# Optimization experiments

Measured on AMD Instinct MI355X. Metric: run time of the kernel, lower is better.

The kernel has to match this reference:

```python
import jax, jax.numpy as jnp
import numpy as np

N, FIN, FOUT, K = 4096, 512, 128, 4
LRELU_ALPHA = 0.2


def setup_inputs() -> dict:
    key = jax.random.key(0)
    k1, k2, k3, k4 = jax.random.split(key, 4)
    x = jax.random.normal(k1, (N, FIN), dtype=jnp.float32)
    # binary adjacency with guaranteed self-loops so every row has a neighbor
    adj = jax.random.randint(k2, (N, N), 0, 2, dtype=jnp.int32)
    adj = jnp.maximum(adj, jnp.eye(N, dtype=jnp.int32))
    # xavier-uniform-ish init for W:(K,FIN,FOUT) and a:(K,2*FOUT,1)
    limW = float(np.sqrt(6.0 / (FIN + FOUT)))
    W = jax.random.uniform(k3, (K, FIN, FOUT), dtype=jnp.float32, minval=-limW, maxval=limW)
    lima = float(np.sqrt(6.0 / (2 * FOUT + 1)))
    a = jax.random.uniform(k4, (K, 2 * FOUT, 1), dtype=jnp.float32, minval=-lima, maxval=lima)
    return {"x": x, "adj": adj, "W": W, "a": a}


def reference(x, adj, W, a):
    # x: [N, Fin], adj: [N, N] int, W: [K, Fin, F'], a: [K, 2F', 1]
    Fout = W.shape[-1]
    h = jnp.einsum('nf,kfo->nko', x, W)          # [N, K, F'] per-head projection
    a_src = a[:, :Fout, 0]                        # [K, F'] acts on h_i
    a_dst = a[:, Fout:, 0]                        # [K, F'] acts on h_j
    # a^T [h_i || h_j] == a_src . h_i + a_dst . h_j  (no O(N^2) concat)
    e_i = jnp.einsum('nko,ko->nk', h, a_src)      # [N, K]
    e_j = jnp.einsum('nko,ko->nk', h, a_dst)      # [N, K]
    scores = e_i[:, :, None] + e_j.T[None, :, :]  # [N, K, N]
    scores = jax.nn.leaky_relu(scores, LRELU_ALPHA)
    mask = (adj != 0)[:, None, :]                 # [N, 1, N]
    scores = jnp.where(mask, scores, -jnp.inf)
    coeffs = jax.nn.softmax(scores, axis=-1)      # [N, K, N]
    # dropout is identity in eval mode
    out = jnp.einsum('nkm,mko->nko', coeffs, h)   # [N, K, F'] aggregation
    return out.reshape(out.shape[0], -1)          # concat heads -> [N, K*F']
```

## Files before the change

kernel.cpp:

```cpp
#include <hip/hip_runtime.h>
#include <hip/hip_bf16.h>

typedef float f4 __attribute__((ext_vector_type(4)));
typedef int   i4 __attribute__((ext_vector_type(4)));
typedef unsigned short us8 __attribute__((ext_vector_type(8)));
typedef short bfrag __attribute__((ext_vector_type(8)));
typedef float f16v __attribute__((ext_vector_type(16)));

constexpr int NN   = 4096;
constexpr int FINc = 512;
constexpr int FOUTc= 128;
constexpr int KHc  = 4;
constexpr int KFc  = 512;
constexpr float ALPHA = 0.2f;
constexpr float LOG2E = 1.44269504088896340736f;

static __device__ __forceinline__ unsigned short f2bf(float f) {
    unsigned u = __float_as_uint(f);
    return (unsigned short)((u + 0x7fffu + ((u >> 16) & 1u)) >> 16);
}
static __device__ __forceinline__ float bf2f(unsigned short u) {
    return __uint_as_float(((unsigned)u) << 16);
}
static __device__ __forceinline__ bfrag us2bf(us8 v) {
    union { us8 u; bfrag s; } cv; cv.u = v; return cv.s;
}


__global__ __launch_bounds__(256) void prep_kernel(const float* __restrict__ x,
                                                   const float* __restrict__ W,
                                                   unsigned short* __restrict__ xb,
                                                   unsigned short* __restrict__ WbT) {
    __shared__ float tile[32 * 132];
    const int b = blockIdx.x, t = threadIdx.x;
    if (b < 1024) {
        size_t base = ((size_t)b * 256 + t) * 8;
        f4 v0 = *(const f4*)&x[base];
        f4 v1 = *(const f4*)&x[base + 4];
        us8 o;
#pragma unroll
        for (int j = 0; j < 4; ++j) { o[j] = f2bf(v0[j]); o[4 + j] = f2bf(v1[j]); }
        *(us8*)&xb[base] = o;
    } else {
        const int wb = b - 1024;
        const int k = wb >> 4, f0 = (wb & 15) * 32;
#pragma unroll
        for (int p = 0; p < 4; ++p) {
            int fl = p * 8 + (t >> 5);
            int oc = (t & 31) * 4;
            *(f4*)&tile[fl * 132 + oc] =
                *(const f4*)&W[(size_t)k * 65536 + (size_t)(f0 + fl) * 128 + oc];
        }
        __syncthreads();
        const int o = t >> 1, fh = (t & 1) * 16;
        alignas(16) unsigned short buf[16];
#pragma unroll
        for (int j = 0; j < 16; ++j) buf[j] = f2bf(tile[(fh + j) * 132 + o]);
        unsigned short* dst = &WbT[((size_t)k * 128 + o) * FINc + f0 + fh];
        *(us8*)dst       = *(const us8*)&buf[0];
        *(us8*)(dst + 8) = *(const us8*)&buf[8];
    }
}

__global__ __launch_bounds__(256) void gemmh_bits_kernel(const unsigned short* __restrict__ xb,
                                                         const unsigned short* __restrict__ WbT,
                                                         const int* __restrict__ adj,
                                                         unsigned short* __restrict__ hB,
                                                         unsigned* __restrict__ bits) {
    __shared__ char Ax[64 * 128];
    __shared__ char Bx[64 * 128];
    const int b = blockIdx.x, t = threadIdx.x;
    if (b >= 512) {
        size_t i0 = (size_t)(b - 512) * 16384 + (size_t)t * 64;
        const int* ap = adj + i0;
        unsigned long long bb = 0ull;
#pragma unroll
        for (int c = 0; c < 16; ++c) {
            i4 v = *(const i4*)(ap + c * 4);
            unsigned n = (v[0] != 0 ? 1u : 0u) | (v[1] != 0 ? 2u : 0u)
                       | (v[2] != 0 ? 4u : 0u) | (v[3] != 0 ? 8u : 0u);
            bb |= (unsigned long long)n << (c * 4);
        }
        *(unsigned long long*)&bits[i0 >> 5] = bb;
        return;
    }
    const int wid = t >> 6, lane = t & 63;
    const int c0 = (b & 7) * 64, n0 = (b >> 3) * 64;
    const int head = c0 >> 7, ob = c0 & 127;
    const int srow = t >> 2, sseg = t & 3;
    const unsigned short* asrc = &xb[(size_t)(n0 + srow) * FINc + sseg * 16];
    const unsigned short* bsrc = &WbT[((size_t)(head * 128 + ob + srow)) * FINc + sseg * 16];
    const int rowbase = (wid & 1) * 32, colbase = (wid >> 1) * 32;
    f16v acc = {};
    for (int fc = 0; fc < FINc; fc += 64) {
        us8 a0 = *(const us8*)(asrc + fc), a1 = *(const us8*)(asrc + fc + 8);
        us8 b0 = *(const us8*)(bsrc + fc), b1 = *(const us8*)(bsrc + fc + 8);
        __syncthreads();
        {
            int byt = (sseg * 32) ^ ((srow & 7) << 4);
            char* pa = Ax + srow * 128;
            *(us8*)(pa + byt) = a0;  *(us8*)(pa + (byt ^ 16)) = a1;
            char* pb = Bx + srow * 128;
            *(us8*)(pb + byt) = b0;  *(us8*)(pb + (byt ^ 16)) = b1;
        }
        __syncthreads();
#pragma unroll
        for (int ks = 0; ks < 4; ++ks) {
            int kb = ks * 32 + ((lane >> 5) << 4);
            int ar = rowbase + (lane & 31);
            bfrag af = *(const bfrag*)(Ax + ar * 128 + (kb ^ ((ar & 7) << 4)));
            int bc = colbase + (lane & 31);
            bfrag bf = *(const bfrag*)(Bx + bc * 128 + (kb ^ ((bc & 7) << 4)));
            acc = __builtin_amdgcn_mfma_f32_32x32x16_bf16(af, bf, acc, 0, 0, 0);
        }
    }
    __syncthreads();
#pragma unroll
    for (int reg = 0; reg < 16; ++reg) {
        int row = rowbase + (reg & 3) + 8 * (reg >> 2) + 4 * (lane >> 5);
        int col = colbase + (lane & 31);
        *(unsigned short*)(Ax + row * 128 + ((col * 2) ^ ((row & 7) << 4))) = f2bf(acc[reg]);
    }
    __syncthreads();
    {
        const int col_l = t & 63;
        unsigned short* dstbase = hB + (size_t)head * 524288 + (size_t)(n0 >> 6) * 8192
                                     + (size_t)(ob + col_l) * 8;
#pragma unroll
        for (int g = 0; g < 2; ++g) {
            int o8 = (t >> 6) + g * 4;
            int ks = o8 >> 1, lg = o8 & 1;
            alignas(16) unsigned short buf[8];
#pragma unroll
            for (int j = 0; j < 8; ++j) {
                int r = o8 * 8 + j;
                buf[j] = *(const unsigned short*)(Ax + r * 128 + ((col_l * 2) ^ ((r & 7) << 4)));
            }
            *(us8*)(dstbase + ks * 2048 + lg * 1024) = *(const us8*)buf;
        }
    }
}

__global__ __launch_bounds__(256) void e2_kernel(const unsigned short* __restrict__ hB,
                                                 const float* __restrict__ a,
                                                 float* __restrict__ ei,
                                                 float* __restrict__ ejT) {
    __shared__ unsigned short hs[8192];
    __shared__ float as[128], ad[128];
    __shared__ float pim[4][64], pjm[4][64];
    const int t = threadIdx.x;
    const int k = blockIdx.x >> 6;
    const int mc = blockIdx.x & 63;
    if (t < 128) as[t] = a[k * 256 + t] * LOG2E;
    else         ad[t - 128] = a[k * 256 + t] * LOG2E;
    const unsigned short* src = hB + ((size_t)k * 64 + mc) * 8192;
#pragma unroll
    for (int i = 0; i < 4; ++i) {
        int off = i * 2048 + t * 8;
        *(us8*)&hs[off] = *(const us8*)&src[off];
    }
    __syncthreads();
    const int m = t & 63, wq = t >> 6;
    const int base = (m >> 4) * 2048 + ((m >> 3) & 1) * 1024 + (m & 7);
    float si = 0.f, sj = 0.f;
#pragma unroll
    for (int cc = 0; cc < 32; ++cc) {
        int c = wq * 32 + cc;
        float v = bf2f(hs[base + c * 8]);
        si += v * as[c];
        sj += v * ad[c];
    }
    pim[wq][m] = si; pjm[wq][m] = sj;
    __syncthreads();
    if (t < 64) {
        ei[(mc * 64 + t) * KHc + k]        = pim[0][t] + pim[1][t] + pim[2][t] + pim[3][t];
        ejT[(size_t)k * NN + mc * 64 + t]  = pjm[0][t] + pjm[1][t] + pjm[2][t] + pjm[3][t];
    }
}

__global__ __launch_bounds__(256, 2) void out_mfma_kernel(const unsigned* __restrict__ bits,
                                                          const float* __restrict__ ei,
                                                          const float* __restrict__ ejT,
                                                          const unsigned short* __restrict__ hB,
                                                          float* __restrict__ out) {
    __shared__ unsigned bitsL[4][1056];
    __shared__ float ejred[4096];
    __shared__ float sred[4][32];
    __shared__ float lsum[32];
    const int bid = blockIdx.x;
    const int nb  = (bid & 7) * 64 + (bid >> 3);
    const int k   = nb >> 7;
    const int n0  = (nb & 127) * 32;
    const int t = threadIdx.x, lane = t & 63, w = t >> 6;
    const int row = lane & 31, kh = lane >> 5;
    const int mq  = w * 1024;
    {
        int r = lane >> 1, cb = (lane & 1) * 16;
        const unsigned* src = &bits[(size_t)(n0 + r) * 128 + (mq >> 5) + cb];
        unsigned* dst = &bitsL[w][r * 33 + cb];
#pragma unroll
        for (int c = 0; c < 16; ++c) dst[c] = src[c];
    }
    {
        const float* src = &ejT[(size_t)k * NN + mq + lane * 16];
        float* dst = &ejred[w * 1024 + lane * 16];
#pragma unroll
        for (int c = 0; c < 4; ++c) *(f4*)(dst + c * 4) = *(const f4*)(src + c * 4);
    }
    const float eiv = ei[(n0 + row) * KHc + k];
    const char* hbase = (const char*)hB + (size_t)k * 1048576 + (size_t)(mq >> 6) * 16384
                        + kh * 2048 + row * 16;
    bfrag ones;
#pragma unroll
    for (int j = 0; j < 8; ++j) ones[j] = (short)0x3F80;
    f16v acc0 = {}, acc1 = {}, acc2 = {}, acc3 = {}, accs = {};

    for (int it = 0; it < 16; ++it) {
        const char* hc = hbase + (size_t)it * 16384;
        unsigned bwA = bitsL[w][row * 33 + it * 2];
        unsigned bwB = bitsL[w][row * 33 + it * 2 + 1];
#pragma unroll
        for (int ks = 0; ks < 4; ++ks) {
            us8 hg0 = *(const us8*)(hc + ks * 4096);
            us8 hg1 = *(const us8*)(hc + ks * 4096 + 512);
            us8 hg2 = *(const us8*)(hc + ks * 4096 + 1024);
            us8 hg3 = *(const us8*)(hc + ks * 4096 + 1536);
            const int eb = w * 1024 + it * 64 + ks * 16 + kh * 8;
            f4 ej0 = *(const f4*)&ejred[eb];
            f4 ej1 = *(const f4*)&ejred[eb + 4];
            unsigned bw = ((ks & 2) ? bwB : bwA) >> ((ks & 1) * 16 + kh * 8);
            float p[8];
#pragma unroll
            for (int j = 0; j < 8; ++j) {
                float sc = eiv + (j < 4 ? ej0[j] : ej1[j - 4]);
                sc = fmaxf(sc, ALPHA * sc);
                float pp = exp2f(sc);
                p[j] = ((bw >> j) & 1) ? pp : 0.f;
            }
            union { unsigned u[4]; bfrag s; } pk;
#pragma unroll
            for (int j = 0; j < 4; ++j) {
                float2 fp; fp.x = p[2 * j]; fp.y = p[2 * j + 1];
                __hip_bfloat162 b2 = __float22bfloat162_rn(fp);
                pk.u[j] = *reinterpret_cast<unsigned*>(&b2);
            }
            acc0 = __builtin_amdgcn_mfma_f32_32x32x16_bf16(pk.s, us2bf(hg0), acc0, 0, 0, 0);
            acc1 = __builtin_amdgcn_mfma_f32_32x32x16_bf16(pk.s, us2bf(hg1), acc1, 0, 0, 0);
            acc2 = __builtin_amdgcn_mfma_f32_32x32x16_bf16(pk.s, us2bf(hg2), acc2, 0, 0, 0);
            acc3 = __builtin_amdgcn_mfma_f32_32x32x16_bf16(pk.s, us2bf(hg3), acc3, 0, 0, 0);
            accs = __builtin_amdgcn_mfma_f32_32x32x16_bf16(pk.s, ones, accs, 0, 0, 0);
        }
    }
    if (row == 0) {
#pragma unroll
        for (int reg = 0; reg < 16; ++reg) {
            int r = (reg & 3) + 8 * (reg >> 2) + 4 * kh;
            sred[w][r] = accs[reg];
        }
    }
    __syncthreads();
    if (t < 32) lsum[t] = 1.0f / ((sred[0][t] + sred[1][t]) + (sred[2][t] + sred[3][t]));
    float* red = ejred;
#pragma unroll
    for (int src = 1; src < 4; ++src) {
        if (w == src) {
#pragma unroll
            for (int cg = 0; cg < 4; ++cg) {
                const f16v& av = (cg == 0) ? acc0 : (cg == 1) ? acc1 : (cg == 2) ? acc2 : acc3;
#pragma unroll
                for (int reg = 0; reg < 16; ++reg) {
                    int r = (reg & 3) + 8 * (reg >> 2) + 4 * kh;
                    red[r * 128 + cg * 32 + row] = av[reg];
                }
            }
        }
        __syncthreads();
        if (w == 0) {
#pragma unroll
            for (int cg = 0; cg < 4; ++cg) {
                f16v& av = (cg == 0) ? acc0 : (cg == 1) ? acc1 : (cg == 2) ? acc2 : acc3;
#pragma unroll
                for (int reg = 0; reg < 16; ++reg) {
                    int r = (reg & 3) + 8 * (reg >> 2) + 4 * kh;
                    av[reg] += red[r * 128 + cg * 32 + row];
                }
            }
        }
        __syncthreads();
    }
    if (w == 0) {
#pragma unroll
        for (int cg = 0; cg < 4; ++cg) {
            const f16v& av = (cg == 0) ? acc0 : (cg == 1) ? acc1 : (cg == 2) ? acc2 : acc3;
#pragma unroll
            for (int reg = 0; reg < 16; ++reg) {
                int r = (reg & 3) + 8 * (reg >> 2) + 4 * kh;
                out[(size_t)(n0 + r) * KFc + k * FOUTc + cg * 32 + row] = av[reg] * lsum[r];
            }
        }
    }
}

extern "C" void kernel_launch(void* const* d_in, const int* in_sizes, int n_in,
                              void* d_out, int out_size, void* d_ws, size_t ws_size,
                              hipStream_t stream) {
    const float* x   = (const float*)d_in[0];
    const int*   adj = (const int*)d_in[1];
    const float* W   = (const float*)d_in[2];
    const float* a   = (const float*)d_in[3];
    float* out = (float*)d_out;
    char* ws = (char*)d_ws;

    unsigned short* hB   = (unsigned short*)ws;
    unsigned short* xb   = (unsigned short*)(ws + (4u << 20));
    unsigned short* WbT  = (unsigned short*)(ws + (20u << 20));
    unsigned*       bits = (unsigned*)(ws + (21u << 20));
    float*          ei   = (float*)(ws + (23u << 20));
    float*          ejT  = ei + (size_t)NN * KHc;

    prep_kernel<<<1088, 256, 0, stream>>>(x, W, xb, WbT);
    gemmh_bits_kernel<<<1536, 256, 0, stream>>>(xb, WbT, adj, hB, bits);
    e2_kernel<<<256, 256, 0, stream>>>(hB, a, ei, ejT);
    out_mfma_kernel<<<512, 256, 0, stream>>>(bits, ei, ejT, hB, out);
}
```

Baseline: 78.53 us.

## Factor leaky-relu exp into precomputed per-column terms and double waves per block

Rewrites exp2(leaky(ei+ej)) as max(exp2(ej), exp2(-0.8*ei)*exp2(0.2*ej)) up to a per-row factor that cancels in normalization. The per-column exponentials are computed once into shared memory, so the inner loop no longer evaluates an exp per element. The block also grows from 4 to 8 waves, each covering half as many columns, to add latency hiding, at the cost of a longer cross-wave reduction and more LDS. The factored form can overflow or lose precision when the ej values are large.

New measurement: 74.05 us. 1.06x faster.

```diff
diff --git a/kernel.cpp b/kernel.cpp
--- a/kernel.cpp
+++ b/kernel.cpp
@@ -12,7 +12,6 @@
 constexpr int FOUTc= 128;
 constexpr int KHc  = 4;
 constexpr int KFc  = 512;
-constexpr float ALPHA = 0.2f;
 constexpr float LOG2E = 1.44269504088896340736f;
 
 static __device__ __forceinline__ unsigned short f2bf(float f) {
@@ -178,14 +177,15 @@
     }
 }
 
-__global__ __launch_bounds__(256, 2) void out_mfma_kernel(const unsigned* __restrict__ bits,
+__global__ __launch_bounds__(512, 4) void out_mfma_kernel(const unsigned* __restrict__ bits,
                                                           const float* __restrict__ ei,
                                                           const float* __restrict__ ejT,
                                                           const unsigned short* __restrict__ hB,
                                                           float* __restrict__ out) {
-    __shared__ unsigned bitsL[4][1056];
-    __shared__ float ejred[4096];
-    __shared__ float sred[4][32];
+    __shared__ unsigned bitsL[8][544];
+    __shared__ float ejPL[4096];
+    __shared__ float ejNL[4096];
+    __shared__ float sred[8][32];
     __shared__ float lsum[32];
     const int bid = blockIdx.x;
     const int nb  = (bid & 7) * 64 + (bid >> 3);
@@ -193,21 +193,30 @@
     const int n0  = (nb & 127) * 32;
     const int t = threadIdx.x, lane = t & 63, w = t >> 6;
     const int row = lane & 31, kh = lane >> 5;
-    const int mq  = w * 1024;
+    const int mq  = w * 512;
     {
-        int r = lane >> 1, cb = (lane & 1) * 16;
+        int r = lane >> 1, cb = (lane & 1) * 8;
         const unsigned* src = &bits[(size_t)(n0 + r) * 128 + (mq >> 5) + cb];
-        unsigned* dst = &bitsL[w][r * 33 + cb];
-#pragma unroll
-        for (int c = 0; c < 16; ++c) dst[c] = src[c];
+        unsigned* dst = &bitsL[w][r * 17 + cb];
+#pragma unroll
+        for (int c = 0; c < 8; ++c) dst[c] = src[c];
     }
     {
-        const float* src = &ejT[(size_t)k * NN + mq + lane * 16];
-        float* dst = &ejred[w * 1024 + lane * 16];
-#pragma unroll
-        for (int c = 0; c < 4; ++c) *(f4*)(dst + c * 4) = *(const f4*)(src + c * 4);
+        const float* src = &ejT[(size_t)k * NN + mq + lane * 8];
+        f4 v0 = *(const f4*)src;
+        f4 v1 = *(const f4*)(src + 4);
+        float* dP = &ejPL[w * 512 + lane * 8];
+        float* dN = &ejNL[w * 512 + lane * 8];
+#pragma unroll
+        for (int c = 0; c < 4; ++c) {
+            dP[c]     = exp2f(v0[c]);
+            dP[c + 4] = exp2f(v1[c]);
+            dN[c]     = exp2f(0.2f * v0[c]);
+            dN[c + 4] = exp2f(0.2f * v1[c]);
+        }
     }
     const float eiv = ei[(n0 + row) * KHc + k];
+    const float C = exp2f(-0.8f * eiv);
     const char* hbase = (const char*)hB + (size_t)k * 1048576 + (size_t)(mq >> 6) * 16384
                         + kh * 2048 + row * 16;
     bfrag ones;
@@ -215,27 +224,29 @@
     for (int j = 0; j < 8; ++j) ones[j] = (short)0x3F80;
     f16v acc0 = {}, acc1 = {}, acc2 = {}, acc3 = {}, accs = {};
 
-    for (int it = 0; it < 16; ++it) {
+    for (int it = 0; it < 8; ++it) {
         const char* hc = hbase + (size_t)it * 16384;
-        unsigned bwA = bitsL[w][row * 33 + it * 2];
-        unsigned bwB = bitsL[w][row * 33 + it * 2 + 1];
+        unsigned bwA = bitsL[w][row * 17 + it * 2];
+        unsigned bwB = bitsL[w][row * 17 + it * 2 + 1];
 #pragma unroll
         for (int ks = 0; ks < 4; ++ks) {
             us8 hg0 = *(const us8*)(hc + ks * 4096);
             us8 hg1 = *(const us8*)(hc + ks * 4096 + 512);
             us8 hg2 = *(const us8*)(hc + ks * 4096 + 1024);
             us8 hg3 = *(const us8*)(hc + ks * 4096 + 1536);
-            const int eb = w * 1024 + it * 64 + ks * 16 + kh * 8;
-            f4 ej0 = *(const f4*)&ejred[eb];
-            f4 ej1 = *(const f4*)&ejred[eb + 4];
+            const int eb = w * 512 + it * 64 + ks * 16 + kh * 8;
+            f4 jp0 = *(const f4*)&ejPL[eb];
+            f4 jp1 = *(const f4*)&ejPL[eb + 4];
+            f4 jn0 = *(const f4*)&ejNL[eb];
+            f4 jn1 = *(const f4*)&ejNL[eb + 4];
             unsigned bw = ((ks & 2) ? bwB : bwA) >> ((ks & 1) * 16 + kh * 8);
             float p[8];
 #pragma unroll
             for (int j = 0; j < 8; ++j) {
-                float sc = eiv + (j < 4 ? ej0[j] : ej1[j - 4]);
-                sc = fmaxf(sc, ALPHA * sc);
-                float pp = exp2f(sc);
-                p[j] = ((bw >> j) & 1) ? pp : 0.f;
+                float jp = (j < 4) ? jp0[j] : jp1[j - 4];
+                float jn = (j < 4) ? jn0[j] : jn1[j - 4];
+                float v = fmaxf(jp, C * jn);
+                p[j] = ((bw >> j) & 1) ? v : 0.f;
             }
             union { unsigned u[4]; bfrag s; } pk;
 #pragma unroll
@@ -259,10 +270,14 @@
         }
     }
     __syncthreads();
-    if (t < 32) lsum[t] = 1.0f / ((sred[0][t] + sred[1][t]) + (sred[2][t] + sred[3][t]));
-    float* red = ejred;
-#pragma unroll
-    for (int src = 1; src < 4; ++src) {
+    if (t < 32) {
+        float s = ((sred[0][t] + sred[1][t]) + (sred[2][t] + sred[3][t]))
+                + ((sred[4][t] + sred[5][t]) + (sred[6][t] + sred[7][t]));
+        lsum[t] = 1.0f / s;
+    }
+    float* red = ejPL;
+#pragma unroll
+    for (int src = 1; src < 8; ++src) {
         if (w == src) {
 #pragma unroll
             for (int cg = 0; cg < 4; ++cg) {
@@ -321,5 +336,5 @@
     prep_kernel<<<1088, 256, 0, stream>>>(x, W, xb, WbT);
     gemmh_bits_kernel<<<1536, 256, 0, stream>>>(xb, WbT, adj, hB, bits);
     e2_kernel<<<256, 256, 0, stream>>>(hB, a, ei, ejT);
-    out_mfma_kernel<<<512, 256, 0, stream>>>(bits, ei, ejT, hB, out);
-}
+    out_mfma_kernel<<<512, 512, 0, stream>>>(bits, ei, ejT, hB, out);
+}
```
